# Performance work log

Measured on AMD Instinct MI355X. Metric: run time of the kernel, lower is better.

The kernel has to match this reference:

```python
import jax, jax.numpy as jnp
import numpy as np

NUM_NODES = 50000
NUM_EDGES = 800000
D_FEAT = 64
NUM_SPECIES = 10


def setup_inputs() -> dict:
    key = jax.random.key(0)
    k1, k2, k3 = jax.random.split(key, 3)
    # edge_center (row 0) sorted by destination node, mimicking AtomicData layout
    edge_center = jnp.sort(jax.random.randint(k1, (NUM_EDGES,), 0, NUM_NODES, dtype=jnp.int64))
    edge_src = jax.random.randint(k2, (NUM_EDGES,), 0, NUM_NODES, dtype=jnp.int64)
    edge_index = jnp.stack([edge_center, edge_src], axis=0)  # [2, E]
    edge_feat = jax.random.normal(k3, (NUM_EDGES, D_FEAT), dtype=jnp.float32)
    node_types = jax.random.randint(jax.random.fold_in(key, 7), (NUM_NODES, 1), 0, NUM_SPECIES, dtype=jnp.int64)
    return {"edge_index": edge_index, "edge_feat": edge_feat, "node_types": node_types}


def reference(edge_index, edge_feat, node_types):
    # EdgewiseReduce.forward: scatter-sum edge features into destination nodes.
    edge_center = edge_index[0]                      # [E]
    num_nodes = node_types.shape[0]                  # len(species)
    out = jax.ops.segment_sum(edge_feat, edge_center, num_segments=num_nodes)  # [N, D]
    return out
```

## Files before the change

### kernel.cpp

```cpp
#include <hip/hip_runtime.h>


#define D_FEAT 64

__global__ void build_offsets_kernel(const int* __restrict__ center,
                                     int* __restrict__ offsets,
                                     int E, int N) {
    int e = blockIdx.x * blockDim.x + threadIdx.x;
    if (e >= E) return;
    int c = center[e];
    int prev = (e == 0) ? -1 : center[e - 1];
    for (int n = prev + 1; n <= c; ++n) offsets[n] = e;
    if (e == E - 1) {
        for (int n = c + 1; n <= N; ++n) offsets[n] = E;
    }
}

__global__ __launch_bounds__(256) void segment_sum_kernel(
        const float* __restrict__ feat,
        const int* __restrict__ offsets,
        float* __restrict__ out, int N) {
    const int wave = threadIdx.x >> 6;
    const int lane = threadIdx.x & 63;
    const int node = blockIdx.x * 4 + wave;
    if (node >= N) return;

    const int start = offsets[node];
    const int deg   = offsets[node + 1] - start;
    const int sub = lane & 15;
    const int grp = lane >> 4;

    int n4 = (deg - grp + 3) >> 2;
    if (n4 < 0) n4 = 0;

    const float* p = feat + (size_t)(start + grp) * D_FEAT + (sub << 2);
    float4 acc = make_float4(0.f, 0.f, 0.f, 0.f);

    while (n4 >= 4) {
        const float4 a0 = *(const float4*)(p);
        const float4 a1 = *(const float4*)(p + 256);
        const float4 a2 = *(const float4*)(p + 512);
        const float4 a3 = *(const float4*)(p + 768);
        acc.x += (a0.x + a1.x) + (a2.x + a3.x);
        acc.y += (a0.y + a1.y) + (a2.y + a3.y);
        acc.z += (a0.z + a1.z) + (a2.z + a3.z);
        acc.w += (a0.w + a1.w) + (a2.w + a3.w);
        p += 1024;
        n4 -= 4;
    }
    if (n4 >= 2) {
        const float4 a0 = *(const float4*)(p);
        const float4 a1 = *(const float4*)(p + 256);
        acc.x += a0.x + a1.x;
        acc.y += a0.y + a1.y;
        acc.z += a0.z + a1.z;
        acc.w += a0.w + a1.w;
        p += 512;
        n4 -= 2;
    }
    if (n4 >= 1) {
        const float4 a0 = *(const float4*)(p);
        acc.x += a0.x; acc.y += a0.y; acc.z += a0.z; acc.w += a0.w;
    }

    #pragma unroll
    for (int m = 32; m >= 16; m >>= 1) {
        acc.x += __shfl_xor(acc.x, m, 64);
        acc.y += __shfl_xor(acc.y, m, 64);
        acc.z += __shfl_xor(acc.z, m, 64);
        acc.w += __shfl_xor(acc.w, m, 64);
    }

    if (grp == 0) {
        *(float4*)(out + (size_t)node * D_FEAT + (sub << 2)) = acc;
    }
}

extern "C" void kernel_launch(void* const* d_in, const int* in_sizes, int n_in,
                              void* d_out, int out_size, void* d_ws, size_t ws_size,
                              hipStream_t stream) {
    const int*   edge_index = (const int*)d_in[0];
    const float* edge_feat  = (const float*)d_in[1];

    const int E = in_sizes[0] / 2;
    const int N = in_sizes[2];

    const int* center = edge_index;
    int* offsets = (int*)d_ws;

    build_offsets_kernel<<<(E + 255) / 256, 256, 0, stream>>>(center, offsets, E, N);
    segment_sum_kernel<<<(N + 3) / 4, 256, 0, stream>>>(edge_feat, offsets,
                                                        (float*)d_out, N);
}
```

Before: 286.5 us.

## Fuse offset construction into segment-sum via wave-parallel 64-ary binary search

Removes the separate build_offsets kernel and workspace offsets array. Each wave instead finds its node's segment start and end with a 64-way parallel search over the sorted center indices, using ballot and popcount. This saves a kernel launch and the offsets write and read. In exchange it adds about three to four dependent global-load rounds per search, two searches per node, to every wave's critical path.

```diff
diff --git a/kernel.cpp b/kernel.cpp
--- a/kernel.cpp
+++ b/kernel.cpp
@@ -3,30 +3,42 @@
 
 #define D_FEAT 64
 
-__global__ void build_offsets_kernel(const int* __restrict__ center,
-                                     int* __restrict__ offsets,
-                                     int E, int N) {
-    int e = blockIdx.x * blockDim.x + threadIdx.x;
-    if (e >= E) return;
-    int c = center[e];
-    int prev = (e == 0) ? -1 : center[e - 1];
-    for (int n = prev + 1; n <= c; ++n) offsets[n] = e;
-    if (e == E - 1) {
-        for (int n = c + 1; n <= N; ++n) offsets[n] = E;
+__device__ __forceinline__ int lower_bound64(const int* __restrict__ center,
+                                             int E, int target, int lane) {
+    int lo = 0, hi = E;
+    while (hi > lo) {
+        const int range = hi - lo;
+        const int s = (range + 63) >> 6;
+        const int p = lo + lane * s;
+        bool pred = false;
+        if (p < hi) pred = (center[p] < target);
+        const unsigned long long m = __ballot(pred);
+        const int c = __popcll(m);
+        if (c == 0) {
+            hi = lo;
+        } else {
+            const int nlo = lo + (c - 1) * s + 1;
+            int nhi = lo + c * s;
+            if (nhi > hi) nhi = hi;
+            lo = nlo; hi = nhi;
+        }
     }
+    return lo;
 }
 
-__global__ __launch_bounds__(256) void segment_sum_kernel(
+__global__ __launch_bounds__(256) void fused_segment_sum_kernel(
+        const int* __restrict__ center,
         const float* __restrict__ feat,
-        const int* __restrict__ offsets,
-        float* __restrict__ out, int N) {
+        float* __restrict__ out, int N, int E) {
     const int wave = threadIdx.x >> 6;
     const int lane = threadIdx.x & 63;
     const int node = blockIdx.x * 4 + wave;
     if (node >= N) return;
 
-    const int start = offsets[node];
-    const int deg   = offsets[node + 1] - start;
+    const int start = lower_bound64(center, E, node, lane);
+    const int end   = lower_bound64(center, E, node + 1, lane);
+    const int deg   = end - start;
+
     const int sub = lane & 15;
     const int grp = lane >> 4;
 
@@ -85,10 +97,6 @@
     const int E = in_sizes[0] / 2;
     const int N = in_sizes[2];
 
-    const int* center = edge_index;
-    int* offsets = (int*)d_ws;
-
-    build_offsets_kernel<<<(E + 255) / 256, 256, 0, stream>>>(center, offsets, E, N);
-    segment_sum_kernel<<<(N + 3) / 4, 256, 0, stream>>>(edge_feat, offsets,
-                                                        (float*)d_out, N);
+    fused_segment_sum_kernel<<<(N + 3) / 4, 256, 0, stream>>>(
+        edge_index , edge_feat, (float*)d_out, N, E);
 }
```

New measurement: 293.6 us. +2.5%, slower.
